# Kernel optimization log

Hardware: AMD Instinct MI355X
Metric: run time of the kernel (lower is better)

## Reference

```python
import jax, jax.numpy as jnp
import numpy as np

B, C, H, W = 4, 96, 48, 48
N_STATE = 16
EXPAND = 2
D_INNER = EXPAND * C          # 192
DT_RANK = -(-C // 16)         # ceil(96/16) = 6
K = 4                         # 4 scan directions (VMamba cross-scan)
CA_R = 16                     # channel-attention reduction


def _ln(x, g, b, eps=1e-5):
    m = jnp.mean(x, -1, keepdims=True)
    v = jnp.mean((x - m) ** 2, -1, keepdims=True)
    return (x - m) * jax.lax.rsqrt(v + eps) * g + b


def setup_inputs() -> dict:
    key = jax.random.key(0)
    ks = jax.random.split(key, 12)
    f = lambda k, s, scale=0.02: jax.random.normal(k, s, dtype=jnp.float32) * scale
    # dt bias init per SS2D.dt_init: inv_dt = dt + log(-expm1(-dt))
    dt0 = jnp.exp(jax.random.uniform(ks[7], (K, D_INNER)) * (np.log(0.1) - np.log(1e-3)) + np.log(1e-3))
    dt_b = dt0 + jnp.log(-jnp.expm1(-dt0))
    A_logs = jnp.log(jnp.tile(jnp.arange(1, N_STATE + 1, dtype=jnp.float32)[None, :], (K * D_INNER, 1)))
    return {
        "x": jax.random.normal(ks[0], (B, C, H, W), dtype=jnp.float32),
        "ca_w1": f(ks[1], (C // CA_R, C), 0.1),
        "ca_w2": f(ks[2], (C, C // CA_R), 0.1),
        "ln_g": jnp.ones((C,), jnp.float32),
        "ln_b": jnp.zeros((C,), jnp.float32),
        "in_proj_w": f(ks[3], (2 * D_INNER, C)),
        "conv_w": f(ks[4], (D_INNER, 1, 3, 3), 0.1),
        "conv_b": jnp.zeros((D_INNER,), jnp.float32),
        "x_proj_w": f(ks[5], (K, DT_RANK + 2 * N_STATE, D_INNER)),
        "dt_w": f(ks[6], (K, D_INNER, DT_RANK), DT_RANK ** -0.5),
        "dt_b": dt_b,
        "A_logs": A_logs,
        "Ds": jnp.ones((K * D_INNER,), jnp.float32),
        "onorm_g": jnp.ones((D_INNER,), jnp.float32),
        "onorm_b": jnp.zeros((D_INNER,), jnp.float32),
        "out_proj_w": f(ks[8], (C, D_INNER)),
    }


def reference(x, ca_w1, ca_w2, ln_g, ln_b, in_proj_w, conv_w, conv_b,
              x_proj_w, dt_w, dt_b, A_logs, Ds, onorm_g, onorm_b, out_proj_w):
    # --- channel attention (SE-style) gating the encoder features ---
    s = x.mean((2, 3))                                    # [B,C]
    a = jax.nn.sigmoid(jax.nn.relu(s @ ca_w1.T) @ ca_w2.T)
    x_ca = x * a[:, :, None, None]

    # --- VSSBlock: LN -> SS2D -> residual ---
    xi = jnp.transpose(x_ca, (0, 2, 3, 1))               # [B,H,W,C]
    xn = _ln(xi, ln_g, ln_b)

    # SS2D in_proj, split x/z
    xz = xn @ in_proj_w.T                                 # [B,H,W,2*D]
    xc, z = jnp.split(xz, 2, axis=-1)

    # depthwise conv + SiLU
    xc = jnp.transpose(xc, (0, 3, 1, 2))                  # [B,D,H,W]
    xc = jax.lax.conv_general_dilated(
        xc, conv_w, (1, 1), 'SAME', feature_group_count=D_INNER,
        dimension_numbers=('NCHW', 'OIHW', 'NCHW')) + conv_b[None, :, None, None]
    xc = jax.nn.silu(xc)

    Bb, D, Hh, Ww = xc.shape
    L = Hh * Ww
    # cross-scan: hw, wh, and their reverses -> [B,4,D,L]
    x_hw = xc.reshape(Bb, D, L)
    x_wh = jnp.transpose(xc, (0, 1, 3, 2)).reshape(Bb, D, L)
    xs = jnp.stack([x_hw, x_wh], axis=1)
    xs = jnp.concatenate([xs, jnp.flip(xs, axis=-1)], axis=1)

    x_dbl = jnp.einsum('bkdl,kcd->bkcl', xs, x_proj_w)    # [B,4,R+2N,L]
    dts, Bs, Cs = jnp.split(x_dbl, [DT_RANK, DT_RANK + N_STATE], axis=2)
    dt = jnp.einsum('bkrl,kdr->bkdl', dts, dt_w)
    dt = jax.nn.softplus(dt + dt_b[None, :, :, None])     # [B,4,D,L]
    A = -jnp.exp(A_logs).reshape(K, D, N_STATE)           # [4,D,N]

    # selective scan over L (sequential recurrence, vectorized over B,K,D,N)
    dt_t = jnp.moveaxis(dt, -1, 0)                        # [L,B,4,D]
    B_t = jnp.moveaxis(Bs, -1, 0)                         # [L,B,4,N]
    C_t = jnp.moveaxis(Cs, -1, 0)
    u_t = jnp.moveaxis(xs, -1, 0)                         # [L,B,4,D]
    h0 = jnp.zeros((Bb, K, D, N_STATE), xc.dtype)

    def step(h, inp):
        dti, Bi, Ci, ui = inp
        h = h * jnp.exp(dti[..., None] * A) + (dti * ui)[..., None] * Bi[:, :, None, :]
        return h, jnp.einsum('bkdn,bkn->bkd', h, Ci)

    _, ys = jax.lax.scan(step, h0, (dt_t, B_t, C_t, u_t))
    ys = jnp.moveaxis(ys, 0, -1) + Ds.reshape(K, D)[None, :, :, None] * xs  # [B,4,D,L]

    # merge 4 directions back to hw order
    y_fwd, y_inv = ys[:, :2], jnp.flip(ys[:, 2:], axis=-1)

    def wh_to_hw(t):
        return jnp.transpose(t.reshape(Bb, D, Ww, Hh), (0, 1, 3, 2)).reshape(Bb, D, L)

    y = y_fwd[:, 0] + y_inv[:, 0] + wh_to_hw(y_fwd[:, 1]) + wh_to_hw(y_inv[:, 1])
    y = jnp.transpose(y.reshape(Bb, D, Hh, Ww), (0, 2, 3, 1))  # [B,H,W,D]
    y = _ln(y, onorm_g, onorm_b)
    y = y * jax.nn.silu(z)
    out = y @ out_proj_w.T                                # [B,H,W,C]
    out = xi + out                                        # VSSBlock residual
    return jnp.transpose(out, (0, 3, 1, 2))               # [B,C,H,W]
```

## Files before the change

kernel.cpp:

```cpp
#include <hip/hip_runtime.h>
#include <math.h>

#define Bn 4
#define Cc 96
#define Hh 48
#define Ww 48
#define HW 2304
#define Dd 192
#define NS 16
#define Kk 4
#define RK 6
#define CD 38
#define Ll 2304
#define NCH 32
#define CL 72
#define SU2S 72

typedef _Float16 half2v __attribute__((ext_vector_type(2)));
typedef _Float16 half4 __attribute__((ext_vector_type(4)));
typedef _Float16 half8 __attribute__((ext_vector_type(8)));
typedef float f4v __attribute__((ext_vector_type(4)));
typedef float f4raw __attribute__((ext_vector_type(4)));

#define FMA4(A,W,U) { A.x=fmaf(W,U.x,A.x); A.y=fmaf(W,U.y,A.y); A.z=fmaf(W,U.z,A.z); A.w=fmaf(W,U.w,A.w); }

__device__ __forceinline__ float sigmoidf_(float x){ return 1.0f/(1.0f+__expf(-x)); }
__device__ __forceinline__ float siluf_(float x){ return x*sigmoidf_(x); }
__device__ __forceinline__ float softplus_fast(float x){ return (x>15.0f)? x : __logf(1.0f+__expf(x)); }

__device__ __forceinline__ float dot2f(half2v a, half2v b, float c){
#if __has_builtin(__builtin_amdgcn_fdot2)
  return __builtin_amdgcn_fdot2(a, b, c, false);
#else
  return fmaf((float)a[1],(float)b[1], fmaf((float)a[0],(float)b[0], c));
#endif
}

__global__ __launch_bounds__(256) void k_mean(const float* __restrict__ x, float* __restrict__ s){
  int bc = blockIdx.x;
  const float* p = x + (size_t)bc*HW;
  float acc = 0.f;
  for(int i=threadIdx.x;i<HW;i+=256) acc += p[i];
  __shared__ float red[256];
  red[threadIdx.x]=acc; __syncthreads();
  for(int o=128;o>0;o>>=1){ if(threadIdx.x<o) red[threadIdx.x]+=red[threadIdx.x+o]; __syncthreads(); }
  if(threadIdx.x==0) s[bc]=red[0]*(1.0f/HW);
}

__global__ __launch_bounds__(384) void k_ca(const float* __restrict__ s, const float* __restrict__ w1,
                     const float* __restrict__ w2, float* __restrict__ a){
  __shared__ float hid[Bn*RK];
  int tid=threadIdx.x;
  if(tid<Bn*RK){
    int b=tid/RK, r=tid%RK;
    float acc=0.f;
    for(int c=0;c<Cc;c++) acc += s[b*Cc+c]*w1[r*Cc+c];
    hid[tid]=fmaxf(acc,0.f);
  }
  __syncthreads();
  int b=tid/Cc, c=tid%Cc;
  float acc=0.f;
  for(int r=0;r<RK;r++) acc += hid[b*RK+r]*w2[c*RK+r];
  a[tid]=sigmoidf_(acc);
}

__global__ __launch_bounds__(256) void k_xca(const float* __restrict__ x, const float* __restrict__ a,
                      float* __restrict__ xi){
  __shared__ float tile[32][65];
  int p0 = blockIdx.x*64, c0 = blockIdx.y*32, b = blockIdx.z;
  int pj = threadIdx.x%64, ci = threadIdx.x/64;
  for(int i=0;i<8;i++){
    int c = c0+ci+i*4;
    tile[ci+i*4][pj] = x[((size_t)(b*Cc+c))*HW + p0+pj]*a[b*Cc+c];
  }
  __syncthreads();
  int cl = threadIdx.x%32, pl = threadIdx.x/32;
  for(int i=0;i<8;i++){
    int p = pl + i*8;
    xi[((size_t)(b*HW + p0+p))*Cc + c0+cl] = tile[cl][p];
  }
}

__global__ __launch_bounds__(256) void k_lnproj(const float* __restrict__ xi,
    const float* __restrict__ g, const float* __restrict__ bta,
    const float* __restrict__ w, float* __restrict__ xc, float* __restrict__ z){
  __shared__ float su[Cc*36];
  __shared__ _Float16 wl16[128*104];
  int tid = threadIdx.x;
  int pix0 = blockIdx.x*32;
  int p = blockIdx.y;
  #pragma unroll
  for(int i=0;i<3;i++){
    int f4 = tid + 256*i;
    int px = f4/24, c4 = f4%24;
    float4 v = *(const float4*)(xi + (size_t)(pix0+px)*Cc + 4*c4);
    int sw = 4*(c4&7);
    su[(4*c4+0)*36 + (px^sw)] = v.x;
    su[(4*c4+1)*36 + (px^sw)] = v.y;
    su[(4*c4+2)*36 + (px^sw)] = v.z;
    su[(4*c4+3)*36 + (px^sw)] = v.w;
  }
  __syncthreads();
  {
    int px = tid>>3, gg = tid&7;
    float sm=0.f, sq=0.f;
    float vals[12];
    #pragma unroll
    for(int i=0;i<12;i++){
      int d = gg + 8*i;
      float v = su[d*36 + (px ^ (4*((d>>2)&7)))];
      vals[i]=v; sm+=v; sq+=v*v;
    }
    sm += __shfl_xor(sm,1); sq += __shfl_xor(sq,1);
    sm += __shfl_xor(sm,2); sq += __shfl_xor(sq,2);
    sm += __shfl_xor(sm,4); sq += __shfl_xor(sq,4);
    float mean = sm*(1.0f/Cc);
    float var  = sq*(1.0f/Cc) - mean*mean;
    float rs = rsqrtf(var + 1e-5f);
    #pragma unroll
    for(int i=0;i<12;i++){
      int d = gg + 8*i;
      su[d*36 + (px ^ (4*((d>>2)&7)))] = (vals[i]-mean)*rs*g[d] + bta[d];
    }
  }
  #pragma unroll
  for(int i=0;i<12;i++){
    int f4 = tid + 256*i;
    int r = f4/24, c4 = f4%24;
    float4 v = *(const float4*)(w + (size_t)(128*p + r)*Cc + 4*c4);
    half4 hv; hv[0]=(_Float16)v.x; hv[1]=(_Float16)v.y; hv[2]=(_Float16)v.z; hv[3]=(_Float16)v.w;
    *(half4*)(wl16 + r*104 + 4*c4) = hv;
  }
  __syncthreads();
  int t4 = tid&7, cg = tid>>3;
  float4 a0={0,0,0,0},a1={0,0,0,0},a2={0,0,0,0},a3={0,0,0,0};
  for(int d0=0; d0<Cc; d0+=8){
    half8 w0v = *(const half8*)(wl16 + (cg+  0)*104 + d0);
    half8 w1v = *(const half8*)(wl16 + (cg+ 32)*104 + d0);
    half8 w2v = *(const half8*)(wl16 + (cg+ 64)*104 + d0);
    half8 w3v = *(const half8*)(wl16 + (cg+ 96)*104 + d0);
    #pragma unroll
    for(int j=0;j<8;j++){
      int d = d0+j;
      float4 u4 = *(const float4*)(su + d*36 + 4*(t4 ^ ((d>>2)&7)));
      FMA4(a0,(float)w0v[j],u4);
      FMA4(a1,(float)w1v[j],u4);
      FMA4(a2,(float)w2v[j],u4);
      FMA4(a3,(float)w3v[j],u4);
    }
  }
  #pragma unroll
  for(int j=0;j<4;j++){
    int c = 128*p + cg + 32*j;
    float4 a = (j==0)?a0:(j==1)?a1:(j==2)?a2:a3;
    #pragma unroll
    for(int q=0;q<4;q++){
      int px = pix0 + 4*t4 + q;
      float vv = (q==0)?a.x:(q==1)?a.y:(q==2)?a.z:a.w;
      if(c < Dd) xc[(size_t)px*Dd + c] = vv;
      else       z [(size_t)px*Dd + (c-Dd)] = vv;
    }
  }
}

__global__ __launch_bounds__(256) void k_conv(const float* __restrict__ xc, const float* __restrict__ cw,
                       const float* __restrict__ cb, float* __restrict__ xo){
  int idx = blockIdx.x*256 + threadIdx.x;
  if(idx >= Bn*HW*(Dd/4)) return;
  int d4 = idx % (Dd/4); int pos = (idx/(Dd/4))%HW; int b = idx/((Dd/4)*HW);
  int h = pos/Ww, w = pos%Ww;
  int d0 = d4*4;
  float4 acc = {cb[d0],cb[d0+1],cb[d0+2],cb[d0+3]};
  #pragma unroll
  for(int kh=0;kh<3;kh++){
    int hh=h+kh-1; if(hh<0||hh>=Hh) continue;
    #pragma unroll
    for(int kw=0;kw<3;kw++){
      int ww2=w+kw-1; if(ww2<0||ww2>=Ww) continue;
      float4 v = *(const float4*)(xc + ((size_t)(b*HW + hh*Ww+ww2))*Dd + d0);
      int wi = kh*3+kw;
      acc.x += v.x*cw[(d0+0)*9+wi];
      acc.y += v.y*cw[(d0+1)*9+wi];
      acc.z += v.z*cw[(d0+2)*9+wi];
      acc.w += v.w*cw[(d0+3)*9+wi];
    }
  }
  float4 o; o.x=siluf_(acc.x); o.y=siluf_(acc.y); o.z=siluf_(acc.z); o.w=siluf_(acc.w);
  *(float4*)(xo + ((size_t)(b*HW+pos))*Dd + d0) = o;
}

__global__ __launch_bounds__(256) void k_xdbl(const float* __restrict__ xconv,
   const float* __restrict__ xpw, const float* __restrict__ dtw,
   const float* __restrict__ dtb, _Float16* __restrict__ dtT,
   _Float16* __restrict__ uT, _Float16* __restrict__ BC){
  __shared__ _Float16 su2[96*SU2S];
  __shared__ _Float16 wl16[CD*200];
  __shared__ float dts[RK*36];
  int tid = threadIdx.x;
  int blk = blockIdx.x;
  int tile = blk % (Ll/32);
  int k    = (blk/(Ll/32))%Kk;
  int b    = blk/((Ll/32)*Kk);
  int ord  = k&1;
  bool rev = (k>=2);
  int t0 = tile*32;
  #pragma unroll
  for(int i=0;i<6;i++){
    int f4 = tid+256*i;
    int r = f4/48, c4 = f4%48;
    int t = t0+r;
    int pos = ord ? ((t%Ww)*Ww + t/Ww) : t;
    float4 v = *(const float4*)(xconv + (size_t)(b*HW+pos)*Dd + 4*c4);
    int dp0 = 2*c4;
    int off = ((r>>2) ^ (c4&7))*8 + (r&3)*2;
    half2v p0; p0[0]=(_Float16)v.x; p0[1]=(_Float16)v.y;
    half2v p1; p1[0]=(_Float16)v.z; p1[1]=(_Float16)v.w;
    *(half2v*)(su2 + dp0*SU2S + off) = p0;
    *(half2v*)(su2 + (dp0+1)*SU2S + off) = p1;
  }
  for(int i=tid;i<CD*48;i+=256){
    int c = i/48, c4 = i%48;
    float4 v = *(const float4*)(xpw + ((size_t)(k*CD+c))*Dd + 4*c4);
    half4 hv; hv[0]=(_Float16)v.x; hv[1]=(_Float16)v.y; hv[2]=(_Float16)v.z; hv[3]=(_Float16)v.w;
    *(half4*)(wl16 + c*200 + 4*c4) = hv;
  }
  __syncthreads();
  if(k<2 && tid < Dd){
    int d = tid;
    int dp = d>>1, par = d&1, swz = (dp>>1)&7;
    _Float16* up = uT + ((size_t)(b*2+ord)*Dd + d)*Ll + t0;
    #pragma unroll
    for(int r4=0;r4<8;r4++){
      half8 hv = *(const half8*)(su2 + dp*SU2S + (r4 ^ swz)*8);
      half4 o; o[0]=hv[0+par]; o[1]=hv[2+par]; o[2]=hv[4+par]; o[3]=hv[6+par];
      *(half4*)(up + 4*r4) = o;
    }
  }
  int t4 = tid&7, cg = tid>>3;
  bool has1 = (cg < CD-32);
  f4v a0={0,0,0,0}, a1={0,0,0,0};
  #pragma unroll 1
  for(int dpc=0; dpc<24; dpc++){
    f4raw w0r = *(const f4raw*)(wl16 + cg*200 + 8*dpc);
    f4raw w1r = {0.f,0.f,0.f,0.f};
    if(has1) w1r = *(const f4raw*)(wl16 + (cg+32)*200 + 8*dpc);
    #pragma unroll
    for(int j=0;j<4;j++){
      int dp = 4*dpc+j;
      f4raw ur = *(const f4raw*)(su2 + dp*SU2S + (t4 ^ ((dp>>1)&7))*8);
      half2v w0p = __builtin_bit_cast(half2v, w0r[j]);
      half2v w1p = __builtin_bit_cast(half2v, w1r[j]);
      #pragma unroll
      for(int q=0;q<4;q++){
        half2v up = __builtin_bit_cast(half2v, ur[q]);
        a0[q] = dot2f(up, w0p, a0[q]);
        if(has1) a1[q] = dot2f(up, w1p, a1[q]);
      }
    }
  }
  #pragma unroll
  for(int j=0;j<2;j++){
    if(j==1 && !has1) break;
    int c = cg + 32*j;
    f4v a = j? a1 : a0;
    if(c < RK){
      dts[c*36 + 4*t4+0]=a[0]; dts[c*36+4*t4+1]=a[1]; dts[c*36+4*t4+2]=a[2]; dts[c*36+4*t4+3]=a[3];
    } else {
      int nn = c - RK;
      _Float16* dst = BC + ((size_t)(b*Kk+k)*Ll)*32 + nn;
      #pragma unroll
      for(int q=0;q<4;q++){
        int t = t0 + 4*t4 + q;
        int tq = rev ? (Ll-1-t) : t;
        dst[(size_t)tq*32] = (_Float16)a[q];
      }
    }
  }
  __syncthreads();
  int tl = tid&31, ds8 = tid>>5;
  #pragma unroll 4
  for(int i=0;i<24;i++){
    int d = ds8 + 8*i;
    float acc = dtb[k*Dd + d];
    #pragma unroll
    for(int r=0;r<RK;r++) acc = fmaf(dtw[((size_t)(k*Dd+d))*RK + r], dts[r*36 + tl], acc);
    acc = softplus_fast(acc);
    int tq = rev ? (Ll-1-t0-tl) : (t0+tl);
    dtT[((size_t)(b*Kk+k)*Dd + d)*Ll + tq] = (_Float16)acc;
  }
}

__global__ __launch_bounds__(768) void k_scan1(const _Float16* __restrict__ dtT,
  const _Float16* __restrict__ uT, const _Float16* __restrict__ BC,
  const float* __restrict__ Alog, float* __restrict__ hloc, float* __restrict__ Pb){
  int blk=blockIdx.x;
  int ch  = blk%NCH;
  int k   = (blk/NCH)%Kk;
  int b   = blk/(NCH*Kk);
  int tid=threadIdx.x;
  int nq = tid&3, d = tid>>2;
  f4v An;
  #pragma unroll
  for(int i=0;i<4;i++) An[i] = -__expf(Alog[((size_t)(k*Dd+d))*NS + 4*nq + i]);
  const _Float16* dp = dtT + ((size_t)(b*Kk+k)*Dd + d)*Ll + ch*CL;
  const _Float16* ub = uT  + ((size_t)(b*2+(k&1))*Dd + d)*Ll;
  const _Float16* bc = BC  + ((size_t)(b*Kk+k)*Ll + ch*CL)*32 + 4*nq;
  bool rev = (k>=2);
  int s0 = ch*CL;
  f4v h = {0,0,0,0};
  float sdt = 0.f;
  for(int tl=0; tl<CL; tl+=4){
    half4 dt4 = *(const half4*)(dp+tl);
    float u[4];
    if(!rev){
      half4 u4 = *(const half4*)(ub + s0+tl);
      u[0]=(float)u4[0]; u[1]=(float)u4[1]; u[2]=(float)u4[2]; u[3]=(float)u4[3];
    } else {
      half4 u4 = *(const half4*)(ub + (Ll-4-s0-tl));
      u[0]=(float)u4[3]; u[1]=(float)u4[2]; u[2]=(float)u4[1]; u[3]=(float)u4[0];
    }
    #pragma unroll
    for(int j=0;j<4;j++){
      half4 Bv = *(const half4*)(bc + (size_t)(tl+j)*32);
      float dtv = (float)dt4[j];
      sdt += dtv;
      float xB = dtv*u[j];
      #pragma unroll
      for(int i=0;i<4;i++){
        float ae = __expf(dtv*An[i]);
        h[i] = fmaf(h[i], ae, xB*(float)Bv[i]);
      }
    }
  }
  size_t o = (((size_t)(b*Kk+k)*NCH + ch)*Dd + d)*NS + 4*nq;
  *(f4v*)(hloc + o) = h;
  f4v P;
  #pragma unroll
  for(int i=0;i<4;i++) P[i] = __expf(An[i]*sdt);
  *(f4v*)(Pb + o) = P;
}

__global__ __launch_bounds__(256) void k_comb(float* __restrict__ hloc,
  const float* __restrict__ Pb){
  int idx = blockIdx.x*256 + threadIdx.x;
  int inner = idx % (Dd*NS);
  int bk = idx / (Dd*NS);
  size_t base = (size_t)bk*NCH*Dd*NS + inner;
  float H = 0.f;
  for(int ch=0; ch<NCH; ch++){
    size_t o = base + (size_t)ch*Dd*NS;
    float hl = hloc[o];
    hloc[o] = H;
    H = Pb[o]*H + hl;
  }
}

__global__ __launch_bounds__(768) void k_scan2(const _Float16* __restrict__ dtT,
  const _Float16* __restrict__ uT, const _Float16* __restrict__ BC,
  const float* __restrict__ Alog, const float* __restrict__ Ds,
  const float* __restrict__ Hin, _Float16* __restrict__ yB){
  int blk=blockIdx.x;
  int ch  = blk%NCH;
  int k   = (blk/NCH)%Kk;
  int b   = blk/(NCH*Kk);
  int tid=threadIdx.x;
  int nq = tid&3, d = tid>>2;
  f4v An;
  #pragma unroll
  for(int i=0;i<4;i++) An[i] = -__expf(Alog[((size_t)(k*Dd+d))*NS + 4*nq + i]);
  float Dv = Ds[k*Dd+d];
  const _Float16* dp = dtT + ((size_t)(b*Kk+k)*Dd + d)*Ll + ch*CL;
  const _Float16* ub = uT  + ((size_t)(b*2+(k&1))*Dd + d)*Ll;
  const _Float16* bc = BC  + ((size_t)(b*Kk+k)*Ll + ch*CL)*32 + 4*nq;
  bool rev = (k>=2);
  int s0 = ch*CL;
  f4v h = *(const f4v*)(Hin + (((size_t)(b*Kk+k)*NCH + ch)*Dd + d)*NS + 4*nq);
  int lane = tid & 63;
  int wv = tid >> 6;
  int src = (lane&15)*4 + (lane>>4);
  _Float16* ybase2 = yB + ((size_t)(b*Kk+k)*Ll + s0 + (lane>>4))*Dd + wv*16 + (lane&15);
  for(int tl=0; tl<CL; tl+=4){
    half4 dt4 = *(const half4*)(dp+tl);
    float u[4];
    if(!rev){
      half4 u4 = *(const half4*)(ub + s0+tl);
      u[0]=(float)u4[0]; u[1]=(float)u4[1]; u[2]=(float)u4[2]; u[3]=(float)u4[3];
    } else {
      half4 u4 = *(const half4*)(ub + (Ll-4-s0-tl));
      u[0]=(float)u4[3]; u[1]=(float)u4[2]; u[2]=(float)u4[1]; u[3]=(float)u4[0];
    }
    float yreg = 0.f;
    #pragma unroll
    for(int j=0;j<4;j++){
      half4 Bv = *(const half4*)(bc + (size_t)(tl+j)*32);
      half4 Cv = *(const half4*)(bc + (size_t)(tl+j)*32 + 16);
      float dtv = (float)dt4[j];
      float xB = dtv*u[j];
      #pragma unroll
      for(int i=0;i<4;i++){
        float ae = __expf(dtv*An[i]);
        h[i] = fmaf(h[i], ae, xB*(float)Bv[i]);
      }
      float p = h[0]*(float)Cv[0];
      p = fmaf(h[1],(float)Cv[1],p); p = fmaf(h[2],(float)Cv[2],p); p = fmaf(h[3],(float)Cv[3],p);
      p += __shfl_xor(p,1); p += __shfl_xor(p,2);
      if(nq==j) yreg = p + Dv*u[j];
    }
    float yout = __shfl(yreg, src);
    ybase2[(size_t)tl*Dd] = (_Float16)yout;
  }
}

__global__ __launch_bounds__(256) void k_merge(const _Float16* __restrict__ yB,
  const float* __restrict__ og, const float* __restrict__ ob,
  const float* __restrict__ zB, const float* __restrict__ opw,
  const float* __restrict__ xi, float* __restrict__ ot){
  __shared__ float yv[Dd*36];
  __shared__ _Float16 wl16[48*200];
  int tid = threadIdx.x;
  int pix0 = blockIdx.x*32;
  int p = blockIdx.y;
  int b = pix0/HW;
  int pos0 = pix0%HW;
  size_t ybase = (size_t)b*Kk*Ll*Dd;
  #pragma unroll
  for(int i=0;i<3;i++){
    int f8 = tid+256*i;
    int r = f8/24, c8 = f8%24;
    int pos = pos0+r;
    int lwh = (pos%Ww)*Ww + pos/Ww;
    half8 v0 = *(const half8*)(yB + ybase + ((size_t)(0*Ll) + pos)*Dd + 8*c8);
    half8 v2 = *(const half8*)(yB + ybase + ((size_t)(2*Ll) + (Ll-1-pos))*Dd + 8*c8);
    half8 v1 = *(const half8*)(yB + ybase + ((size_t)(1*Ll) + lwh)*Dd + 8*c8);
    half8 v3 = *(const half8*)(yB + ybase + ((size_t)(3*Ll) + (Ll-1-lwh))*Dd + 8*c8);
    #pragma unroll
    for(int j=0;j<8;j++){
      int d = 8*c8+j;
      float vs = (float)v0[j]+(float)v1[j]+(float)v2[j]+(float)v3[j];
      yv[d*36 + (r ^ (4*((d>>2)&7)))] = vs;
    }
  }
  for(int i=tid;i<48*48;i+=256){
    int c=i/48, c4=i%48;
    float4 v = *(const float4*)(opw + (size_t)(48*p+c)*Dd + 4*c4);
    half4 hv; hv[0]=(_Float16)v.x; hv[1]=(_Float16)v.y; hv[2]=(_Float16)v.z; hv[3]=(_Float16)v.w;
    *(half4*)(wl16 + c*200 + 4*c4) = hv;
  }
  __syncthreads();
  {
    int px = tid>>3, gg = tid&7;
    float sm=0.f, sq=0.f;
    float vals[24];
    #pragma unroll
    for(int i=0;i<24;i++){
      int d = gg + 8*i;
      float v = yv[d*36 + (px ^ (4*((d>>2)&7)))];
      vals[i]=v; sm+=v; sq+=v*v;
    }
    sm += __shfl_xor(sm,1); sq += __shfl_xor(sq,1);
    sm += __shfl_xor(sm,2); sq += __shfl_xor(sq,2);
    sm += __shfl_xor(sm,4); sq += __shfl_xor(sq,4);
    float mean = sm*(1.0f/Dd);
    float var  = sq*(1.0f/Dd) - mean*mean;
    float rs = rsqrtf(var + 1e-5f);
    #pragma unroll
    for(int i=0;i<24;i++){
      int d = gg + 8*i;
      float zv = zB[(size_t)(pix0+px)*Dd + d];
      yv[d*36 + (px ^ (4*((d>>2)&7)))] = ((vals[i]-mean)*rs*og[d] + ob[d]) * siluf_(zv);
    }
  }
  __syncthreads();
  int t4 = tid&7, cg = tid>>3;
  bool h1 = (cg < 16);
  float4 a0={0,0,0,0}, a1={0,0,0,0};
  for(int d0=0;d0<Dd;d0+=8){
    half8 w0v = *(const half8*)(wl16 + cg*200 + d0);
    half8 w1v;
    if(h1) w1v = *(const half8*)(wl16 + (cg+32)*200 + d0);
    #pragma unroll
    for(int j=0;j<8;j++){
      int d=d0+j;
      float4 u4 = *(const float4*)(yv + d*36 + 4*(t4 ^ ((d>>2)&7)));
      FMA4(a0,(float)w0v[j],u4);
      if(h1){ FMA4(a1,(float)w1v[j],u4); }
    }
  }
  #pragma unroll
  for(int j=0;j<2;j++){
    if(j==1 && !h1) break;
    int c = 48*p + cg + 32*j;
    float4 a = j?a1:a0;
    #pragma unroll
    for(int q=0;q<4;q++){
      int px = pix0 + 4*t4 + q;
      float vv = (q==0)?a.x:(q==1)?a.y:(q==2)?a.z:a.w;
      ot[(size_t)px*Cc + c] = vv + xi[(size_t)px*Cc + c];
    }
  }
}

__global__ __launch_bounds__(256) void k_outT(const float* __restrict__ ot, float* __restrict__ out){
  __shared__ float tile[64][33];
  int p0=blockIdx.x*64, c0=blockIdx.y*32, b=blockIdx.z;
  int cl=threadIdx.x%32, pl=threadIdx.x/32;
  for(int i=0;i<8;i++){
    int p = pl+i*8;
    tile[p][cl] = ot[((size_t)(b*HW+p0+p))*Cc + c0+cl];
  }
  __syncthreads();
  int pj=threadIdx.x%64, ci=threadIdx.x/64;
  for(int i=0;i<8;i++){
    int c=ci+i*4;
    out[((size_t)(b*Cc+c0+c))*HW + p0+pj] = tile[pj][c];
  }
}

extern "C" void kernel_launch(void* const* d_in, const int* in_sizes, int n_in,
                              void* d_out, int out_size, void* d_ws, size_t ws_size,
                              hipStream_t stream){
  const float* x   = (const float*)d_in[0];
  const float* cw1 = (const float*)d_in[1];
  const float* cw2 = (const float*)d_in[2];
  const float* lng = (const float*)d_in[3];
  const float* lnb = (const float*)d_in[4];
  const float* ipw = (const float*)d_in[5];
  const float* cvw = (const float*)d_in[6];
  const float* cvb = (const float*)d_in[7];
  const float* xpw = (const float*)d_in[8];
  const float* dtw = (const float*)d_in[9];
  const float* dtb = (const float*)d_in[10];
  const float* alg = (const float*)d_in[11];
  const float* ds  = (const float*)d_in[12];
  const float* ong = (const float*)d_in[13];
  const float* onb = (const float*)d_in[14];
  const float* opw = (const float*)d_in[15];
  float* out = (float*)d_out;
  float* ws = (float*)d_ws;

  float* s_   = ws;
  float* a_   = s_  + 384;
  float* xi_  = a_  + 384;
  float* xc_  = xi_ + 884736;
  float* z_   = xc_ + 1769472;
  float* xo_  = z_  + 1769472;
  _Float16* dtT_ = (_Float16*)(xo_ + 1769472);
  _Float16* uT_  = dtT_ + 7077888;
  _Float16* BC_  = uT_ + 3538944;
  _Float16* yB_  = BC_ + 1179648;
  float* ot_  = (float*)(yB_ + 7077888);

  float* hloc_ = xc_;
  float* Pb_   = xo_;

  k_mean  <<<Bn*Cc, 256, 0, stream>>>(x, s_);
  k_ca    <<<1, 384, 0, stream>>>(s_, cw1, cw2, a_);
  k_xca   <<<dim3(HW/64, Cc/32, Bn), 256, 0, stream>>>(x, a_, xi_);
  k_lnproj<<<dim3(Bn*HW/32, 3), 256, 0, stream>>>(xi_, lng, lnb, ipw, xc_, z_);
  k_conv  <<<(Bn*HW*(Dd/4))/256, 256, 0, stream>>>(xc_, cvw, cvb, xo_);
  k_xdbl  <<<Bn*Kk*(Ll/32), 256, 0, stream>>>(xo_, xpw, dtw, dtb, dtT_, uT_, BC_);
  k_scan1 <<<Bn*Kk*NCH, 768, 0, stream>>>(dtT_, uT_, BC_, alg, hloc_, Pb_);
  k_comb  <<<(Bn*Kk*Dd*NS)/256, 256, 0, stream>>>(hloc_, Pb_);
  k_scan2 <<<Bn*Kk*NCH, 768, 0, stream>>>(dtT_, uT_, BC_, alg, ds, hloc_, yB_);
  k_merge <<<dim3(Bn*HW/32, 2), 256, 0, stream>>>(yB_, ong, onb, z_, opw, xi_, ot_);
  k_outT  <<<dim3(HW/64, Cc/32, Bn), 256, 0, stream>>>(ot_, out);
}
```

Measured before the change: 189.3 us.

## Assign all 16 SSM states to one thread per channel in scan kernels

Both chunked scan kernels now use one thread per channel d that holds all 16 states in registers, replacing four threads per channel each holding four states. This drops the cross-lane shuffle reduction and the shuffle-based output transpose in scan2, and loads B/C as wider half8 vectors. The cost is a 4x smaller block (192 threads), a 4x lower total thread count over the same 512 blocks, and more registers per thread. That reduces occupancy and latency hiding on a scan that is largely bound by serial exp/FMA work.

Measured after the change: 196.6 us. +3.9%, slower.

```diff
diff --git a/kernel.cpp b/kernel.cpp
--- a/kernel.cpp
+++ b/kernel.cpp
@@ -290,25 +290,28 @@
   }
 }
 
-__global__ __launch_bounds__(768) void k_scan1(const _Float16* __restrict__ dtT,
+__global__ __launch_bounds__(192) void k_scan1(const _Float16* __restrict__ dtT,
   const _Float16* __restrict__ uT, const _Float16* __restrict__ BC,
   const float* __restrict__ Alog, float* __restrict__ hloc, float* __restrict__ Pb){
   int blk=blockIdx.x;
   int ch  = blk%NCH;
   int k   = (blk/NCH)%Kk;
   int b   = blk/(NCH*Kk);
-  int tid=threadIdx.x;
-  int nq = tid&3, d = tid>>2;
-  f4v An;
-  #pragma unroll
-  for(int i=0;i<4;i++) An[i] = -__expf(Alog[((size_t)(k*Dd+d))*NS + 4*nq + i]);
+  int d = threadIdx.x;
+  const float* ap = Alog + ((size_t)(k*Dd+d))*NS;
+  float An[16];
+  #pragma unroll
+  for(int i=0;i<16;i++) An[i] = -__expf(ap[i]);
   const _Float16* dp = dtT + ((size_t)(b*Kk+k)*Dd + d)*Ll + ch*CL;
   const _Float16* ub = uT  + ((size_t)(b*2+(k&1))*Dd + d)*Ll;
-  const _Float16* bc = BC  + ((size_t)(b*Kk+k)*Ll + ch*CL)*32 + 4*nq;
+  const _Float16* bc = BC  + ((size_t)(b*Kk+k)*Ll + ch*CL)*32;
   bool rev = (k>=2);
   int s0 = ch*CL;
-  f4v h = {0,0,0,0};
+  float h[16];
+  #pragma unroll
+  for(int i=0;i<16;i++) h[i]=0.f;
   float sdt = 0.f;
+  #pragma unroll 1
   for(int tl=0; tl<CL; tl+=4){
     half4 dt4 = *(const half4*)(dp+tl);
     float u[4];
@@ -321,23 +324,33 @@
     }
     #pragma unroll
     for(int j=0;j<4;j++){
-      half4 Bv = *(const half4*)(bc + (size_t)(tl+j)*32);
+      half8 B0 = *(const half8*)(bc + (size_t)(tl+j)*32);
+      half8 B1 = *(const half8*)(bc + (size_t)(tl+j)*32 + 8);
       float dtv = (float)dt4[j];
       sdt += dtv;
       float xB = dtv*u[j];
       #pragma unroll
-      for(int i=0;i<4;i++){
+      for(int i=0;i<8;i++){
         float ae = __expf(dtv*An[i]);
-        h[i] = fmaf(h[i], ae, xB*(float)Bv[i]);
+        h[i] = fmaf(h[i], ae, xB*(float)B0[i]);
       }
-    }
-  }
-  size_t o = (((size_t)(b*Kk+k)*NCH + ch)*Dd + d)*NS + 4*nq;
-  *(f4v*)(hloc + o) = h;
-  f4v P;
-  #pragma unroll
-  for(int i=0;i<4;i++) P[i] = __expf(An[i]*sdt);
-  *(f4v*)(Pb + o) = P;
+      #pragma unroll
+      for(int i=0;i<8;i++){
+        float ae = __expf(dtv*An[8+i]);
+        h[8+i] = fmaf(h[8+i], ae, xB*(float)B1[i]);
+      }
+    }
+  }
+  size_t o = (((size_t)(b*Kk+k)*NCH + ch)*Dd + d)*NS;
+  f4v h0={h[0],h[1],h[2],h[3]}, h1={h[4],h[5],h[6],h[7]};
+  f4v h2={h[8],h[9],h[10],h[11]}, h3={h[12],h[13],h[14],h[15]};
+  *(f4v*)(hloc+o)=h0; *(f4v*)(hloc+o+4)=h1; *(f4v*)(hloc+o+8)=h2; *(f4v*)(hloc+o+12)=h3;
+  float P[16];
+  #pragma unroll
+  for(int i=0;i<16;i++) P[i] = __expf(An[i]*sdt);
+  f4v p0={P[0],P[1],P[2],P[3]}, p1={P[4],P[5],P[6],P[7]};
+  f4v p2={P[8],P[9],P[10],P[11]}, p3={P[12],P[13],P[14],P[15]};
+  *(f4v*)(Pb+o)=p0; *(f4v*)(Pb+o+4)=p1; *(f4v*)(Pb+o+8)=p2; *(f4v*)(Pb+o+12)=p3;
 }
 
 __global__ __launch_bounds__(256) void k_comb(float* __restrict__ hloc,
@@ -355,7 +368,7 @@
   }
 }
 
-__global__ __launch_bounds__(768) void k_scan2(const _Float16* __restrict__ dtT,
+__global__ __launch_bounds__(192) void k_scan2(const _Float16* __restrict__ dtT,
   const _Float16* __restrict__ uT, const _Float16* __restrict__ BC,
   const float* __restrict__ Alog, const float* __restrict__ Ds,
   const float* __restrict__ Hin, _Float16* __restrict__ yB){
@@ -363,22 +376,28 @@
   int ch  = blk%NCH;
   int k   = (blk/NCH)%Kk;
   int b   = blk/(NCH*Kk);
-  int tid=threadIdx.x;
-  int nq = tid&3, d = tid>>2;
-  f4v An;
-  #pragma unroll
-  for(int i=0;i<4;i++) An[i] = -__expf(Alog[((size_t)(k*Dd+d))*NS + 4*nq + i]);
+  int d = threadIdx.x;
+  const float* ap = Alog + ((size_t)(k*Dd+d))*NS;
+  float An[16];
+  #pragma unroll
+  for(int i=0;i<16;i++) An[i] = -__expf(ap[i]);
   float Dv = Ds[k*Dd+d];
   const _Float16* dp = dtT + ((size_t)(b*Kk+k)*Dd + d)*Ll + ch*CL;
   const _Float16* ub = uT  + ((size_t)(b*2+(k&1))*Dd + d)*Ll;
-  const _Float16* bc = BC  + ((size_t)(b*Kk+k)*Ll + ch*CL)*32 + 4*nq;
+  const _Float16* bc = BC  + ((size_t)(b*Kk+k)*Ll + ch*CL)*32;
   bool rev = (k>=2);
   int s0 = ch*CL;
-  f4v h = *(const f4v*)(Hin + (((size_t)(b*Kk+k)*NCH + ch)*Dd + d)*NS + 4*nq);
-  int lane = tid & 63;
-  int wv = tid >> 6;
-  int src = (lane&15)*4 + (lane>>4);
-  _Float16* ybase2 = yB + ((size_t)(b*Kk+k)*Ll + s0 + (lane>>4))*Dd + wv*16 + (lane&15);
+  const float* hp = Hin + (((size_t)(b*Kk+k)*NCH + ch)*Dd + d)*NS;
+  float h[16];
+  {
+    f4v h0=*(const f4v*)(hp), h1=*(const f4v*)(hp+4), h2=*(const f4v*)(hp+8), h3=*(const f4v*)(hp+12);
+    h[0]=h0[0];h[1]=h0[1];h[2]=h0[2];h[3]=h0[3];
+    h[4]=h1[0];h[5]=h1[1];h[6]=h1[2];h[7]=h1[3];
+    h[8]=h2[0];h[9]=h2[1];h[10]=h2[2];h[11]=h2[3];
+    h[12]=h3[0];h[13]=h3[1];h[14]=h3[2];h[15]=h3[3];
+  }
+  _Float16* yp = yB + ((size_t)(b*Kk+k)*Ll + s0)*Dd + d;
+  #pragma unroll 1
   for(int tl=0; tl<CL; tl+=4){
     half4 dt4 = *(const half4*)(dp+tl);
     float u[4];
@@ -389,25 +408,29 @@
       half4 u4 = *(const half4*)(ub + (Ll-4-s0-tl));
       u[0]=(float)u4[3]; u[1]=(float)u4[2]; u[2]=(float)u4[1]; u[3]=(float)u4[0];
     }
-    float yreg = 0.f;
     #pragma unroll
     for(int j=0;j<4;j++){
-      half4 Bv = *(const half4*)(bc + (size_t)(tl+j)*32);
-      half4 Cv = *(const half4*)(bc + (size_t)(tl+j)*32 + 16);
+      half8 B0 = *(const half8*)(bc + (size_t)(tl+j)*32);
+      half8 B1 = *(const half8*)(bc + (size_t)(tl+j)*32 + 8);
+      half8 C0 = *(const half8*)(bc + (size_t)(tl+j)*32 + 16);
+      half8 C1 = *(const half8*)(bc + (size_t)(tl+j)*32 + 24);
       float dtv = (float)dt4[j];
       float xB = dtv*u[j];
+      float p = 0.f;
       #pragma unroll
-      for(int i=0;i<4;i++){
+      for(int i=0;i<8;i++){
         float ae = __expf(dtv*An[i]);
-        h[i] = fmaf(h[i], ae, xB*(float)Bv[i]);
+        h[i] = fmaf(h[i], ae, xB*(float)B0[i]);
+        p = fmaf(h[i], (float)C0[i], p);
       }
-      float p = h[0]*(float)Cv[0];
-      p = fmaf(h[1],(float)Cv[1],p); p = fmaf(h[2],(float)Cv[2],p); p = fmaf(h[3],(float)Cv[3],p);
-      p += __shfl_xor(p,1); p += __shfl_xor(p,2);
-      if(nq==j) yreg = p + Dv*u[j];
-    }
-    float yout = __shfl(yreg, src);
-    ybase2[(size_t)tl*Dd] = (_Float16)yout;
+      #pragma unroll
+      for(int i=0;i<8;i++){
+        float ae = __expf(dtv*An[8+i]);
+        h[8+i] = fmaf(h[8+i], ae, xB*(float)B1[i]);
+        p = fmaf(h[8+i], (float)C1[i], p);
+      }
+      yp[(size_t)(tl+j)*Dd] = (_Float16)(p + Dv*u[j]);
+    }
   }
 }
 
@@ -559,9 +582,9 @@
   k_lnproj<<<dim3(Bn*HW/32, 3), 256, 0, stream>>>(xi_, lng, lnb, ipw, xc_, z_);
   k_conv  <<<(Bn*HW*(Dd/4))/256, 256, 0, stream>>>(xc_, cvw, cvb, xo_);
   k_xdbl  <<<Bn*Kk*(Ll/32), 256, 0, stream>>>(xo_, xpw, dtw, dtb, dtT_, uT_, BC_);
-  k_scan1 <<<Bn*Kk*NCH, 768, 0, stream>>>(dtT_, uT_, BC_, alg, hloc_, Pb_);
+  k_scan1 <<<Bn*Kk*NCH, 192, 0, stream>>>(dtT_, uT_, BC_, alg, hloc_, Pb_);
   k_comb  <<<(Bn*Kk*Dd*NS)/256, 256, 0, stream>>>(hloc_, Pb_);
-  k_scan2 <<<Bn*Kk*NCH, 768, 0, stream>>>(dtT_, uT_, BC_, alg, ds, hloc_, yB_);
+  k_scan2 <<<Bn*Kk*NCH, 192, 0, stream>>>(dtT_, uT_, BC_, alg, ds, hloc_, yB_);
   k_merge <<<dim3(Bn*HW/32, 2), 256, 0, stream>>>(yB_, ong, onb, z_, opw, xi_, ot_);
   k_outT  <<<dim3(HW/64, Cc/32, Bn), 256, 0, stream>>>(ot_, out);
 }
```
